# Performance work log

Hardware: AMD Instinct MI355X
Metric: run time of the kernel (lower is better)

## Reference

```python
import jax, jax.numpy as jnp
import numpy as np

B, T, D, H = 2, 2048, 1024, 16
HD = D // H
REG = 16
WIN = 256
ROPE_BASE = 10000.0


def _rope_cos_sin(t, hd):
    theta = 1.0 / (ROPE_BASE ** (jnp.arange(0, hd, 2, dtype=jnp.float32) / hd))  # [hd/2]
    idx_theta = jnp.arange(t, dtype=jnp.float32)[:, None] * theta[None, :]       # [T, hd/2]
    return jnp.cos(idx_theta), jnp.sin(idx_theta)


def _apply_rope(x, cos, sin):
    # x: [B, T, H, HD]
    xs = x.reshape(*x.shape[:-1], HD // 2, 2)
    x0, x1 = xs[..., 0], xs[..., 1]
    c = cos[None, :, None, :]
    s = sin[None, :, None, :]
    out = jnp.stack([x0 * c - x1 * s, x1 * c + x0 * s], axis=-1)
    return out.reshape(x.shape)


def _keep_mask(t):
    # Faithful to _build_attention_register_mask: True = attend (SDPA bool semantics).
    i = jnp.arange(t)[:, None]
    j = jnp.arange(t)[None, :]
    half = WIN // 2
    window_block = (i >= REG) & (j >= jnp.maximum(REG, i - half)) & (j <= i + half)
    blocked = (j < REG) | (i < REG) | window_block
    return ~blocked  # [T, T] bool


def setup_inputs() -> dict:
    key = jax.random.key(0)
    k1, k2, k3 = jax.random.split(key, 3)
    x = jax.random.normal(k1, (B, T, D), dtype=jnp.float32)
    w_attn = jax.random.normal(k2, (3 * D, D), dtype=jnp.float32) * 0.02  # torch Linear weight [out,in]
    w_proj = jax.random.normal(k3, (D, D), dtype=jnp.float32) * 0.02
    return {"x": x, "w_attn": w_attn, "w_proj": w_proj}


def reference(x, w_attn, w_proj):
    b, t, d = x.shape
    qkv = jnp.einsum('btd,ed->bte', x, w_attn)               # [B,T,3D]
    q, k, v = jnp.split(qkv, 3, axis=-1)
    q = q.reshape(b, t, H, HD)
    k = k.reshape(b, t, H, HD)
    v = v.reshape(b, t, H, HD)
    cos, sin = _rope_cos_sin(t, HD)
    q = _apply_rope(q, cos, sin)
    k = _apply_rope(k, cos, sin)
    q = q.transpose(0, 2, 1, 3)  # [B,H,T,HD]
    k = k.transpose(0, 2, 1, 3)
    v = v.transpose(0, 2, 1, 3)
    keep = _keep_mask(t)
    scores = jnp.einsum('bhqd,bhkd->bhqk', q, k) / jnp.sqrt(jnp.float32(HD))
    scores = jnp.where(keep[None, None], scores, -jnp.inf)
    # safe softmax (fully-masked rows -> 0, matching SDPA efficient backends)
    m = jnp.max(scores, axis=-1, keepdims=True)
    m = jnp.where(jnp.isfinite(m), m, 0.0)
    e = jnp.exp(scores - m)
    s = jnp.sum(e, axis=-1, keepdims=True)
    probs = e / jnp.maximum(s, 1e-20)
    y = jnp.einsum('bhqk,bhkd->bhqd', probs, v)
    y = y.transpose(0, 2, 1, 3).reshape(b, t, d)
    return jnp.einsum('btd,ed->bte', y, w_proj)
```

## Files before the change

### kernel.cpp

```cpp
#include <hip/hip_runtime.h>
#include <hip/hip_bf16.h>

#define DEV static __device__ __forceinline__

typedef __attribute__((ext_vector_type(8))) short bf16x8;
typedef __attribute__((ext_vector_type(4))) float f32x4;

#define MFMA16(a, b, c) __builtin_amdgcn_mfma_f32_16x16x32_bf16((a), (b), (c), 0, 0, 0)

#define B_ 2
#define T_ 2048
#define D_ 1024
#define H_ 16
#define HD_ 64
#define LOG2E 1.4426950408889634f

DEV short f2bf(float f) {
  union { float f; unsigned u; } w; w.f = f;
  unsigned u = w.u + 0x7fffu + ((w.u >> 16) & 1u);
  return (short)(u >> 16);
}

DEV void gld16(const void* g, void* l) {
  __builtin_amdgcn_global_load_lds(
      (const __attribute__((address_space(1))) void*)g,
      (__attribute__((address_space(3))) void*)l, 16, 0, 0);
}

#define XN 4194304
#define WAN 3145728
__global__ void cvt_k(const float* __restrict__ x, const float* __restrict__ wa,
                      const float* __restrict__ wp, short* __restrict__ xb,
                      short* __restrict__ wab, short* __restrict__ wpb) {
  size_t gi = ((size_t)blockIdx.x * 256 + threadIdx.x) * 8;
  const float* src; short* dst;
  if (gi < XN) { src = x + gi; dst = xb + gi; }
  else if (gi < XN + WAN) { src = wa + (gi - XN); dst = wab + (gi - XN); }
  else { src = wp + (gi - XN - WAN); dst = wpb + (gi - XN - WAN); }
  float4 a = *(const float4*)src;
  float4 b = *(const float4*)(src + 4);
  bf16x8 o;
  o[0] = f2bf(a.x); o[1] = f2bf(a.y); o[2] = f2bf(a.z); o[3] = f2bf(a.w);
  o[4] = f2bf(b.x); o[5] = f2bf(b.y); o[6] = f2bf(b.z); o[7] = f2bf(b.w);
  *(bf16x8*)dst = o;
}

__global__ void rope_table_k(float2* __restrict__ tab) {
  int i = blockIdx.x * 256 + threadIdx.x;
  if (i >= T_ * 32) return;
  int t = i >> 5, d = i & 31;
  float theta = powf(10000.0f, -(float)(2 * d) / 64.0f);
  float a = (float)t * theta;
  tab[i] = make_float2(cosf(a), sinf(a));
}

#define GEMM_CORE(Aptr, Bptr, KDIM)                                              \
  __shared__ short aT[128 * 64];                                                 \
  __shared__ short bT[128 * 64];                                                 \
  const int tid = threadIdx.x;                                                   \
  const int lane = tid & 63, w = tid >> 6;                                       \
  const int l15 = lane & 15, lg = lane >> 4;                                     \
  const int wr = w >> 1, wc = w & 1;                                             \
  const int mBase = blockIdx.y * 128, nBase = blockIdx.x * 128;                  \
  const int lrow = lane >> 3;                                                    \
  const int gch = (lane & 7) ^ lrow;                                             \
  const short* Asrc = (Aptr) + (size_t)(mBase + w * 32 + lrow) * (KDIM) + gch * 8;\
  const short* Bsrc = (Bptr) + (size_t)(nBase + w * 32 + lrow) * (KDIM) + gch * 8;\
  short* aDst = aT + w * 2048;                                                   \
  short* bDst = bT + w * 2048;                                                   \
  f32x4 acc[4][4];                                                               \
  _Pragma("unroll") for (int i = 0; i < 4; ++i)                                  \
  _Pragma("unroll") for (int j = 0; j < 4; ++j)                                  \
      acc[i][j] = (f32x4){0.f, 0.f, 0.f, 0.f};                                   \
  const int nk = (KDIM) / 64;                                                    \
  for (int kt = 0; kt < nk; ++kt) {                                              \
    if (kt) __syncthreads();                                                     \
    _Pragma("unroll") for (int p = 0; p < 4; ++p) {                              \
      gld16(Asrc + kt * 64 + p * 8 * (KDIM), aDst + p * 512);                    \
      gld16(Bsrc + kt * 64 + p * 8 * (KDIM), bDst + p * 512);                    \
    }                                                                            \
    __syncthreads();                \
    bf16x8 af[4][2], bfv[4][2];                                                  \
    _Pragma("unroll") for (int i = 0; i < 4; ++i)                                \
    _Pragma("unroll") for (int s = 0; s < 2; ++s) {                              \
      const int ra = wr * 64 + i * 16 + l15;                                     \
      const int rb = wc * 64 + i * 16 + l15;                                     \
      af[i][s] = *(const bf16x8*)&aT[ra * 64 + (((4 * s + lg) ^ (ra & 7)) * 8)]; \
      bfv[i][s] = *(const bf16x8*)&bT[rb * 64 + (((4 * s + lg) ^ (rb & 7)) * 8)];\
    }                                                                            \
    _Pragma("unroll") for (int mi = 0; mi < 4; ++mi)                             \
    _Pragma("unroll") for (int ni = 0; ni < 4; ++ni)                             \
    _Pragma("unroll") for (int s = 0; s < 2; ++s)                                \
        acc[mi][ni] = MFMA16(af[mi][s], bfv[ni][s], acc[mi][ni]);                \
  }

__global__ void gemm_qkv_k(const short* __restrict__ Xb, const short* __restrict__ Wb,
                           short* __restrict__ Q, short* __restrict__ Ko,
                           short* __restrict__ Vt, const float2* __restrict__ tab) {
  GEMM_CORE(Xb, Wb, 1024)

  const int sec = nBase >> 10;
#pragma unroll
  for (int mi = 0; mi < 4; ++mi) {
    const int m0 = mBase + wr * 64 + mi * 16 + lg * 4;
#pragma unroll
    for (int ni = 0; ni < 4; ++ni) {
      const int n = nBase + wc * 64 + ni * 16 + l15;
      const int hd = n & 63;
      const int h = (n >> 6) & 15;
      if (sec < 2) {
        short* dst = (sec == 0) ? Q : Ko;
        const float qscale = (sec == 0) ? (0.125f * LOG2E) : 1.0f;
#pragma unroll
        for (int r = 0; r < 4; ++r) {
          int m = m0 + r; int b = m >> 11; int t = m & 2047;
          float v = acc[mi][ni][r];
          float pv = __shfl_xor(v, 1);
          float2 cs = tab[t * 32 + (hd >> 1)];
          float o = (lane & 1) ? (v * cs.x + pv * cs.y) : (v * cs.x - pv * cs.y);
          o *= qscale;
          dst[(((size_t)b * H_ + h) * T_ + t) * HD_ + hd] = f2bf(o);
        }
      } else {
        int b = m0 >> 11; int t0 = m0 & 2047;
        short4 s4;
        s4.x = f2bf(acc[mi][ni][0]); s4.y = f2bf(acc[mi][ni][1]);
        s4.z = f2bf(acc[mi][ni][2]); s4.w = f2bf(acc[mi][ni][3]);
        *(short4*)&Vt[(((size_t)b * H_ + h) * HD_ + hd) * T_ + t0] = s4;
      }
    }
  }
}

__global__ void attn_k(const short* __restrict__ Qg, const short* __restrict__ Kg,
                       const short* __restrict__ Vg, short* __restrict__ Y) {
  __shared__ short kLds[64 * 72];
  __shared__ short vLds[64 * 72];
  __shared__ short pLds[64 * 72];
  const int tid = threadIdx.x;
  const int lane = tid & 63, w = tid >> 6;
  const int l15 = lane & 15, lg = lane >> 4;
  const int bid = blockIdx.x;
  const int wg = ((bid & 7) << 7) | (bid >> 3);
  const int qt = wg & 31, bh = wg >> 5;
  const int b = bh >> 4, h = bh & 15;
  const int q0 = qt * 64;
  const short* Qh = Qg + (size_t)bh * T_ * HD_;
  const short* Kh = Kg + (size_t)bh * T_ * HD_;
  const short* Vh = Vg + (size_t)bh * HD_ * T_;

  bf16x8 qa[2];
  {
    const int qrow = q0 + w * 16 + l15;
    qa[0] = *(const bf16x8*)&Qh[(size_t)qrow * HD_ + lg * 8];
    qa[1] = *(const bf16x8*)&Qh[(size_t)qrow * HD_ + 32 + lg * 8];
  }
  f32x4 o[4];
#pragma unroll
  for (int i = 0; i < 4; ++i) o[i] = (f32x4){0.f, 0.f, 0.f, 0.f};
  float lsum[4] = {0.f, 0.f, 0.f, 0.f};

  const int sRow = tid >> 3, sC = (tid & 7) * 8;
  bf16x8 kreg[2], vreg[2];
  auto issueLoad = [&](int kt) {
    const int k0 = kt * 64;
#pragma unroll
    for (int p = 0; p < 2; ++p) {
      const int row = sRow + p * 32;
      kreg[p] = *(const bf16x8*)&Kh[(size_t)(k0 + row) * HD_ + sC];
      vreg[p] = *(const bf16x8*)&Vh[(size_t)row * T_ + k0 + sC];
    }
  };
  auto inBand = [&](int kt) { const int k0 = kt * 64; return k0 >= q0 - 65 && k0 <= q0 + 65; };

  const int NT = T_ / 64;
  int kt = 0;
  while (kt < NT && inBand(kt)) ++kt;
  issueLoad(kt);

  while (kt < NT) {
    int ktn = kt + 1;
    while (ktn < NT && inBand(ktn)) ++ktn;

    __syncthreads();
#pragma unroll
    for (int p = 0; p < 2; ++p) {
      *(bf16x8*)&kLds[(sRow + p * 32) * 72 + sC] = kreg[p];
      *(bf16x8*)&vLds[(sRow + p * 32) * 72 + sC] = vreg[p];
    }
    if (ktn < NT) issueLoad(ktn);
    asm volatile("s_waitcnt lgkmcnt(0)" ::: "memory");
    __builtin_amdgcn_s_barrier();

    const int k0 = kt * 64;
    const bool clean = (q0 >= 16) && (k0 >= 16) &&
                       ((k0 + 63 < q0 - 128) || (k0 > q0 + 63 + 128));

    f32x4 s[4];
#pragma unroll
    for (int i = 0; i < 4; ++i) s[i] = (f32x4){0.f, 0.f, 0.f, 0.f};
#pragma unroll
    for (int nf = 0; nf < 4; ++nf)
#pragma unroll
      for (int ks = 0; ks < 2; ++ks) {
        bf16x8 kb = *(const bf16x8*)&kLds[(nf * 16 + l15) * 72 + ks * 32 + lg * 8];
        s[nf] = MFMA16(qa[ks], kb, s[nf]);
      }

    if (!clean) {
#pragma unroll
      for (int nf = 0; nf < 4; ++nf) {
        const int j = k0 + nf * 16 + l15;
#pragma unroll
        for (int r = 0; r < 4; ++r) {
          const int i = q0 + w * 16 + lg * 4 + r;
          const bool keep = (i >= 16) && (j >= 16) && ((j < i - 128) || (j > i + 128));
          if (!keep) s[nf][r] = -__builtin_inff();
        }
      }
    }

#pragma unroll
    for (int nf = 0; nf < 4; ++nf)
#pragma unroll
      for (int r = 0; r < 4; ++r) {
        float e = __builtin_amdgcn_exp2f(s[nf][r]);
        lsum[r] += e;
        pLds[(w * 16 + lg * 4 + r) * 72 + nf * 16 + l15] = f2bf(e);
      }
#pragma unroll
    for (int nf = 0; nf < 4; ++nf)
#pragma unroll
      for (int ks = 0; ks < 2; ++ks) {
        bf16x8 pa = *(const bf16x8*)&pLds[(w * 16 + l15) * 72 + ks * 32 + lg * 8];
        bf16x8 vb = *(const bf16x8*)&vLds[(nf * 16 + l15) * 72 + ks * 32 + lg * 8];
        o[nf] = MFMA16(pa, vb, o[nf]);
      }
    kt = ktn;
  }

  float rl[4];
#pragma unroll
  for (int r = 0; r < 4; ++r) {
    float v = lsum[r];
    v += __shfl_xor(v, 1);
    v += __shfl_xor(v, 2);
    v += __shfl_xor(v, 4);
    v += __shfl_xor(v, 8);
    rl[r] = 1.0f / fmaxf(v, 1e-20f);
  }
#pragma unroll
  for (int nf = 0; nf < 4; ++nf)
#pragma unroll
    for (int r = 0; r < 4; ++r) {
      const int t = q0 + w * 16 + lg * 4 + r;
      Y[((size_t)(b * T_ + t)) * D_ + h * HD_ + nf * 16 + l15] = f2bf(o[nf][r] * rl[r]);
    }
}

__global__ void gemm_proj_k(const short* __restrict__ Yg, const short* __restrict__ Wb,
                            float* __restrict__ Out) {
  GEMM_CORE(Yg, Wb, 1024)

#pragma unroll
  for (int mi = 0; mi < 4; ++mi)
#pragma unroll
    for (int ni = 0; ni < 4; ++ni)
#pragma unroll
      for (int r = 0; r < 4; ++r)
        Out[(size_t)(mBase + wr * 64 + mi * 16 + lg * 4 + r) * 1024 +
            nBase + wc * 64 + ni * 16 + l15] = acc[mi][ni][r];
}

extern "C" void kernel_launch(void* const* d_in, const int* in_sizes, int n_in,
                              void* d_out, int out_size, void* d_ws, size_t ws_size,
                              hipStream_t stream) {
  const float* x = (const float*)d_in[0];
  const float* w_attn = (const float*)d_in[1];
  const float* w_proj = (const float*)d_in[2];
  float* out = (float*)d_out;
  char* ws = (char*)d_ws;
  char* outc = (char*)d_out;
  short* Q   = (short*)(ws);
  short* K   = (short*)(ws + (size_t)8388608);
  short* Vt  = (short*)(ws + (size_t)16777216);
  short* Y   = (short*)(ws + (size_t)25165824);
  short* Wpb = (short*)(ws + (size_t)33554432);
  short* Xb   = (short*)(outc);
  short* Wab  = (short*)(outc + (size_t)8388608);
  float2* tab = (float2*)(outc + (size_t)14680064);

  cvt_k<<<dim3(4096), dim3(256), 0, stream>>>(x, w_attn, w_proj, Xb, Wab, Wpb);
  rope_table_k<<<dim3(256), dim3(256), 0, stream>>>(tab);
  gemm_qkv_k<<<dim3(24, 32), dim3(256), 0, stream>>>(Xb, Wab, Q, K, Vt, tab);
  attn_k<<<dim3(B_ * H_ * (T_ / 64)), dim3(256), 0, stream>>>(Q, K, Vt, Y);
  gemm_proj_k<<<dim3(8, 32), dim3(256), 0, stream>>>(Y, Wpb, out);
}
```

Measured before the change: 144.5 us.

## Process 128 query rows per attention block to reuse K/V tiles

Each attention workgroup now handles two 64-row query chunks, so every K/V tile staged in shared memory is used by both chunks and global K/V traffic per query drops by half. The launch grid is halved to match, and the band-skip test is narrowed so only tiles fully masked for both chunks are skipped; partly masked tiles are computed and masked instead. MFMA sections are wrapped in s_setprio raises, and launch bounds request two blocks per CU. The trade is more registers per thread, fewer workgroups to spread across CUs, and some extra masked tile work near the diagonal band.

Result: slower. 148.7 us (+2.9%).

```diff
diff --git a/kernel.cpp b/kernel.cpp
--- a/kernel.cpp
+++ b/kernel.cpp
@@ -132,8 +132,11 @@
   }
 }
 
-__global__ void attn_k(const short* __restrict__ Qg, const short* __restrict__ Kg,
-                       const short* __restrict__ Vg, short* __restrict__ Y) {
+#define QB 128
+__global__ __launch_bounds__(256, 2) void attn_k(const short* __restrict__ Qg,
+                                                 const short* __restrict__ Kg,
+                                                 const short* __restrict__ Vg,
+                                                 short* __restrict__ Y) {
   __shared__ short kLds[64 * 72];
   __shared__ short vLds[64 * 72];
   __shared__ short pLds[64 * 72];
@@ -141,24 +144,31 @@
   const int lane = tid & 63, w = tid >> 6;
   const int l15 = lane & 15, lg = lane >> 4;
   const int bid = blockIdx.x;
-  const int wg = ((bid & 7) << 7) | (bid >> 3);
-  const int qt = wg & 31, bh = wg >> 5;
+  const int wg = ((bid & 7) << 6) | (bid >> 3);
+  const int qt = wg & 15, bh = wg >> 4;
   const int b = bh >> 4, h = bh & 15;
-  const int q0 = qt * 64;
+  const int q0 = qt * QB;
   const short* Qh = Qg + (size_t)bh * T_ * HD_;
   const short* Kh = Kg + (size_t)bh * T_ * HD_;
   const short* Vh = Vg + (size_t)bh * HD_ * T_;
 
-  bf16x8 qa[2];
-  {
-    const int qrow = q0 + w * 16 + l15;
-    qa[0] = *(const bf16x8*)&Qh[(size_t)qrow * HD_ + lg * 8];
-    qa[1] = *(const bf16x8*)&Qh[(size_t)qrow * HD_ + 32 + lg * 8];
-  }
-  f32x4 o[4];
-#pragma unroll
-  for (int i = 0; i < 4; ++i) o[i] = (f32x4){0.f, 0.f, 0.f, 0.f};
-  float lsum[4] = {0.f, 0.f, 0.f, 0.f};
+  bf16x8 qa[2][2];
+#pragma unroll
+  for (int c = 0; c < 2; ++c) {
+    const int qrow = q0 + c * 64 + w * 16 + l15;
+    qa[c][0] = *(const bf16x8*)&Qh[(size_t)qrow * HD_ + lg * 8];
+    qa[c][1] = *(const bf16x8*)&Qh[(size_t)qrow * HD_ + 32 + lg * 8];
+  }
+  f32x4 o[2][4];
+#pragma unroll
+  for (int c = 0; c < 2; ++c)
+#pragma unroll
+    for (int i = 0; i < 4; ++i) o[c][i] = (f32x4){0.f, 0.f, 0.f, 0.f};
+  float lsum[2][4];
+#pragma unroll
+  for (int c = 0; c < 2; ++c)
+#pragma unroll
+    for (int r = 0; r < 4; ++r) lsum[c][r] = 0.f;
 
   const int sRow = tid >> 3, sC = (tid & 7) * 8;
   bf16x8 kreg[2], vreg[2];
@@ -171,7 +181,7 @@
       vreg[p] = *(const bf16x8*)&Vh[(size_t)row * T_ + k0 + sC];
     }
   };
-  auto inBand = [&](int kt) { const int k0 = kt * 64; return k0 >= q0 - 65 && k0 <= q0 + 65; };
+  auto inBand = [&](int kt) { const int k0 = kt * 64; return k0 >= q0 - 1 && k0 <= q0 + 65; };
 
   const int NT = T_ / 64;
   int kt = 0;
@@ -193,69 +203,81 @@
     __builtin_amdgcn_s_barrier();
 
     const int k0 = kt * 64;
-    const bool clean = (q0 >= 16) && (k0 >= 16) &&
-                       ((k0 + 63 < q0 - 128) || (k0 > q0 + 63 + 128));
-
-    f32x4 s[4];
-#pragma unroll
-    for (int i = 0; i < 4; ++i) s[i] = (f32x4){0.f, 0.f, 0.f, 0.f};
+#pragma unroll
+    for (int c = 0; c < 2; ++c) {
+      const int qc = q0 + c * 64;
+      const bool clean = (qc >= 16) && (k0 >= 16) &&
+                         ((k0 + 63 < qc - 128) || (k0 > qc + 63 + 128));
+
+      f32x4 s[4];
+#pragma unroll
+      for (int i = 0; i < 4; ++i) s[i] = (f32x4){0.f, 0.f, 0.f, 0.f};
+      __builtin_amdgcn_s_setprio(1);
+#pragma unroll
+      for (int nf = 0; nf < 4; ++nf)
+#pragma unroll
+        for (int ks = 0; ks < 2; ++ks) {
+          bf16x8 kb = *(const bf16x8*)&kLds[(nf * 16 + l15) * 72 + ks * 32 + lg * 8];
+          s[nf] = MFMA16(qa[c][ks], kb, s[nf]);
+        }
+      __builtin_amdgcn_s_setprio(0);
+
+      if (!clean) {
+#pragma unroll
+        for (int nf = 0; nf < 4; ++nf) {
+          const int j = k0 + nf * 16 + l15;
+#pragma unroll
+          for (int r = 0; r < 4; ++r) {
+            const int i = qc + w * 16 + lg * 4 + r;
+            const bool keep = (i >= 16) && (j >= 16) && ((j < i - 128) || (j > i + 128));
+            if (!keep) s[nf][r] = -__builtin_inff();
+          }
+        }
+      }
+
+#pragma unroll
+      for (int nf = 0; nf < 4; ++nf)
+#pragma unroll
+        for (int r = 0; r < 4; ++r) {
+          float e = __builtin_amdgcn_exp2f(s[nf][r]);
+          lsum[c][r] += e;
+          pLds[(w * 16 + lg * 4 + r) * 72 + nf * 16 + l15] = f2bf(e);
+        }
+      __builtin_amdgcn_s_setprio(1);
+#pragma unroll
+      for (int nf = 0; nf < 4; ++nf)
+#pragma unroll
+        for (int ks = 0; ks < 2; ++ks) {
+          bf16x8 pa = *(const bf16x8*)&pLds[(w * 16 + l15) * 72 + ks * 32 + lg * 8];
+          bf16x8 vb = *(const bf16x8*)&vLds[(nf * 16 + l15) * 72 + ks * 32 + lg * 8];
+          o[c][nf] = MFMA16(pa, vb, o[c][nf]);
+        }
+      __builtin_amdgcn_s_setprio(0);
+    }
+    kt = ktn;
+  }
+
+#pragma unroll
+  for (int c = 0; c < 2; ++c) {
+    float rl[4];
+#pragma unroll
+    for (int r = 0; r < 4; ++r) {
+      float v = lsum[c][r];
+      v += __shfl_xor(v, 1);
+      v += __shfl_xor(v, 2);
+      v += __shfl_xor(v, 4);
+      v += __shfl_xor(v, 8);
+      rl[r] = 1.0f / fmaxf(v, 1e-20f);
+    }
 #pragma unroll
     for (int nf = 0; nf < 4; ++nf)
 #pragma unroll
-      for (int ks = 0; ks < 2; ++ks) {
-        bf16x8 kb = *(const bf16x8*)&kLds[(nf * 16 + l15) * 72 + ks * 32 + lg * 8];
-        s[nf] = MFMA16(qa[ks], kb, s[nf]);
+      for (int r = 0; r < 4; ++r) {
+        const int t = q0 + c * 64 + w * 16 + lg * 4 + r;
+        Y[((size_t)(b * T_ + t)) * D_ + h * HD_ + nf * 16 + l15] =
+            f2bf(o[c][nf][r] * rl[r]);
       }
-
-    if (!clean) {
-#pragma unroll
-      for (int nf = 0; nf < 4; ++nf) {
-        const int j = k0 + nf * 16 + l15;
-#pragma unroll
-        for (int r = 0; r < 4; ++r) {
-          const int i = q0 + w * 16 + lg * 4 + r;
-          const bool keep = (i >= 16) && (j >= 16) && ((j < i - 128) || (j > i + 128));
-          if (!keep) s[nf][r] = -__builtin_inff();
-        }
-      }
-    }
-
-#pragma unroll
-    for (int nf = 0; nf < 4; ++nf)
-#pragma unroll
-      for (int r = 0; r < 4; ++r) {
-        float e = __builtin_amdgcn_exp2f(s[nf][r]);
-        lsum[r] += e;
-        pLds[(w * 16 + lg * 4 + r) * 72 + nf * 16 + l15] = f2bf(e);
-      }
-#pragma unroll
-    for (int nf = 0; nf < 4; ++nf)
-#pragma unroll
-      for (int ks = 0; ks < 2; ++ks) {
-        bf16x8 pa = *(const bf16x8*)&pLds[(w * 16 + l15) * 72 + ks * 32 + lg * 8];
-        bf16x8 vb = *(const bf16x8*)&vLds[(nf * 16 + l15) * 72 + ks * 32 + lg * 8];
-        o[nf] = MFMA16(pa, vb, o[nf]);
-      }
-    kt = ktn;
-  }
-
-  float rl[4];
-#pragma unroll
-  for (int r = 0; r < 4; ++r) {
-    float v = lsum[r];
-    v += __shfl_xor(v, 1);
-    v += __shfl_xor(v, 2);
-    v += __shfl_xor(v, 4);
-    v += __shfl_xor(v, 8);
-    rl[r] = 1.0f / fmaxf(v, 1e-20f);
-  }
-#pragma unroll
-  for (int nf = 0; nf < 4; ++nf)
-#pragma unroll
-    for (int r = 0; r < 4; ++r) {
-      const int t = q0 + w * 16 + lg * 4 + r;
-      Y[((size_t)(b * T_ + t)) * D_ + h * HD_ + nf * 16 + l15] = f2bf(o[nf][r] * rl[r]);
-    }
+  }
 }
 
 __global__ void gemm_proj_k(const short* __restrict__ Yg, const short* __restrict__ Wb,
@@ -293,6 +315,6 @@
   cvt_k<<<dim3(4096), dim3(256), 0, stream>>>(x, w_attn, w_proj, Xb, Wab, Wpb);
   rope_table_k<<<dim3(256), dim3(256), 0, stream>>>(tab);
   gemm_qkv_k<<<dim3(24, 32), dim3(256), 0, stream>>>(Xb, Wab, Q, K, Vt, tab);
-  attn_k<<<dim3(B_ * H_ * (T_ / 64)), dim3(256), 0, stream>>>(Q, K, Vt, Y);
+  attn_k<<<dim3(B_ * H_ * (T_ / QB)), dim3(256), 0, stream>>>(Q, K, Vt, Y);
   gemm_proj_k<<<dim3(8, 32), dim3(256), 0, stream>>>(Y, Wpb, out);
 }
```

## Compute transposed scores to keep P in registers and drop P LDS round-trip

Applied to the files above, without the earlier changes.

The attention kernel now computes S^T (K as the A operand, Q as the B operand), so each lane holds probabilities for one query row in the layout a 16x16x16 bf16 MFMA B operand needs. P then feeds the PV product straight from registers, which removes the pLds buffer and its write/read round trip. The K LDS tile gets an XOR swizzle to cut bank conflicts, and s_setprio is placed around the MFMA sections. The output is staged through LDS to produce coalesced 16-byte stores. The cost is twice as many PV MFMAs at half the K depth, plus an occupancy hint via launch bounds.

New measurement: 149.3 us. 1.03x slower.

```diff
diff --git a/kernel.cpp b/kernel.cpp
--- a/kernel.cpp
+++ b/kernel.cpp
@@ -4,9 +4,23 @@
 #define DEV static __device__ __forceinline__
 
 typedef __attribute__((ext_vector_type(8))) short bf16x8;
+typedef __attribute__((ext_vector_type(4))) short bf16x4;
 typedef __attribute__((ext_vector_type(4))) float f32x4;
 
 #define MFMA16(a, b, c) __builtin_amdgcn_mfma_f32_16x16x32_bf16((a), (b), (c), 0, 0, 0)
+
+DEV f32x4 pv_mfma(bf16x4 a, bf16x4 b, f32x4 c) {
+#if __has_builtin(__builtin_amdgcn_mfma_f32_16x16x16_bf16)
+  return __builtin_amdgcn_mfma_f32_16x16x16_bf16(a, b, c, 0, 0, 0);
+#elif __has_builtin(__builtin_amdgcn_mfma_f32_16x16x16bf16_1k)
+  return __builtin_amdgcn_mfma_f32_16x16x16bf16_1k(a, b, c, 0, 0, 0);
+#else
+  f32x4 d;
+  asm volatile("v_mfma_f32_16x16x16_bf16 %0, %1, %2, %3"
+               : "=v"(d) : "v"(a), "v"(b), "v"(c));
+  return d;
+#endif
+}
 
 #define B_ 2
 #define T_ 2048
@@ -132,11 +146,12 @@
   }
 }
 
-__global__ void attn_k(const short* __restrict__ Qg, const short* __restrict__ Kg,
-                       const short* __restrict__ Vg, short* __restrict__ Y) {
+__global__ __launch_bounds__(256, 4) void attn_k(const short* __restrict__ Qg,
+                                                 const short* __restrict__ Kg,
+                                                 const short* __restrict__ Vg,
+                                                 short* __restrict__ Y) {
   __shared__ short kLds[64 * 72];
   __shared__ short vLds[64 * 72];
-  __shared__ short pLds[64 * 72];
   const int tid = threadIdx.x;
   const int lane = tid & 63, w = tid >> 6;
   const int l15 = lane & 15, lg = lane >> 4;
@@ -149,16 +164,16 @@
   const short* Kh = Kg + (size_t)bh * T_ * HD_;
   const short* Vh = Vg + (size_t)bh * HD_ * T_;
 
-  bf16x8 qa[2];
+  bf16x8 qb[2];
   {
     const int qrow = q0 + w * 16 + l15;
-    qa[0] = *(const bf16x8*)&Qh[(size_t)qrow * HD_ + lg * 8];
-    qa[1] = *(const bf16x8*)&Qh[(size_t)qrow * HD_ + 32 + lg * 8];
-  }
-  f32x4 o[4];
-#pragma unroll
-  for (int i = 0; i < 4; ++i) o[i] = (f32x4){0.f, 0.f, 0.f, 0.f};
-  float lsum[4] = {0.f, 0.f, 0.f, 0.f};
+    qb[0] = *(const bf16x8*)&Qh[(size_t)qrow * HD_ + lg * 8];
+    qb[1] = *(const bf16x8*)&Qh[(size_t)qrow * HD_ + 32 + lg * 8];
+  }
+  f32x4 ot[4];
+#pragma unroll
+  for (int i = 0; i < 4; ++i) ot[i] = (f32x4){0.f, 0.f, 0.f, 0.f};
+  float lsum = 0.f;
 
   const int sRow = tid >> 3, sC = (tid & 7) * 8;
   bf16x8 kreg[2], vreg[2];
@@ -185,8 +200,9 @@
     __syncthreads();
 #pragma unroll
     for (int p = 0; p < 2; ++p) {
-      *(bf16x8*)&kLds[(sRow + p * 32) * 72 + sC] = kreg[p];
-      *(bf16x8*)&vLds[(sRow + p * 32) * 72 + sC] = vreg[p];
+      const int row = sRow + p * 32;
+      *(bf16x8*)&kLds[row * 72 + (((tid & 7) ^ (row & 7)) * 8)] = kreg[p];
+      *(bf16x8*)&vLds[row * 72 + sC] = vreg[p];
     }
     if (ktn < NT) issueLoad(ktn);
     asm volatile("s_waitcnt lgkmcnt(0)" ::: "memory");
@@ -199,63 +215,73 @@
     f32x4 s[4];
 #pragma unroll
     for (int i = 0; i < 4; ++i) s[i] = (f32x4){0.f, 0.f, 0.f, 0.f};
+    __builtin_amdgcn_s_setprio(1);
 #pragma unroll
     for (int nf = 0; nf < 4; ++nf)
 #pragma unroll
       for (int ks = 0; ks < 2; ++ks) {
-        bf16x8 kb = *(const bf16x8*)&kLds[(nf * 16 + l15) * 72 + ks * 32 + lg * 8];
-        s[nf] = MFMA16(qa[ks], kb, s[nf]);
+        const int row = nf * 16 + l15;
+        bf16x8 ka = *(const bf16x8*)&kLds[row * 72 + (((ks * 4 + lg) ^ (row & 7)) * 8)];
+        s[nf] = MFMA16(ka, qb[ks], s[nf]);
       }
-
-    if (!clean) {
-#pragma unroll
-      for (int nf = 0; nf < 4; ++nf) {
-        const int j = k0 + nf * 16 + l15;
-#pragma unroll
-        for (int r = 0; r < 4; ++r) {
-          const int i = q0 + w * 16 + lg * 4 + r;
-          const bool keep = (i >= 16) && (j >= 16) && ((j < i - 128) || (j > i + 128));
+    __builtin_amdgcn_s_setprio(0);
+
+    const int i_q = q0 + w * 16 + l15;
+    bf16x4 pf[4];
+#pragma unroll
+    for (int nf = 0; nf < 4; ++nf)
+#pragma unroll
+      for (int r = 0; r < 4; ++r) {
+        if (!clean) {
+          const int j = k0 + nf * 16 + lg * 4 + r;
+          const bool keep = (i_q >= 16) && (j >= 16) &&
+                            ((j < i_q - 128) || (j > i_q + 128));
           if (!keep) s[nf][r] = -__builtin_inff();
         }
+        float e = __builtin_amdgcn_exp2f(s[nf][r]);
+        lsum += e;
+        pf[nf][r] = f2bf(e);
       }
+
+    __builtin_amdgcn_s_setprio(1);
+#pragma unroll
+    for (int kk = 0; kk < 4; ++kk) {
+      bf16x4 va[4];
+#pragma unroll
+      for (int dt = 0; dt < 4; ++dt)
+        va[dt] = *(const bf16x4*)&vLds[(dt * 16 + l15) * 72 + kk * 16 + lg * 4];
+#pragma unroll
+      for (int dt = 0; dt < 4; ++dt)
+        ot[dt] = pv_mfma(va[dt], pf[kk], ot[dt]);
     }
-
-#pragma unroll
-    for (int nf = 0; nf < 4; ++nf)
-#pragma unroll
-      for (int r = 0; r < 4; ++r) {
-        float e = __builtin_amdgcn_exp2f(s[nf][r]);
-        lsum[r] += e;
-        pLds[(w * 16 + lg * 4 + r) * 72 + nf * 16 + l15] = f2bf(e);
-      }
-#pragma unroll
-    for (int nf = 0; nf < 4; ++nf)
-#pragma unroll
-      for (int ks = 0; ks < 2; ++ks) {
-        bf16x8 pa = *(const bf16x8*)&pLds[(w * 16 + l15) * 72 + ks * 32 + lg * 8];
-        bf16x8 vb = *(const bf16x8*)&vLds[(nf * 16 + l15) * 72 + ks * 32 + lg * 8];
-        o[nf] = MFMA16(pa, vb, o[nf]);
-      }
+    __builtin_amdgcn_s_setprio(0);
     kt = ktn;
   }
 
-  float rl[4];
-#pragma unroll
-  for (int r = 0; r < 4; ++r) {
-    float v = lsum[r];
-    v += __shfl_xor(v, 1);
-    v += __shfl_xor(v, 2);
-    v += __shfl_xor(v, 4);
-    v += __shfl_xor(v, 8);
-    rl[r] = 1.0f / fmaxf(v, 1e-20f);
-  }
-#pragma unroll
-  for (int nf = 0; nf < 4; ++nf)
-#pragma unroll
-    for (int r = 0; r < 4; ++r) {
-      const int t = q0 + w * 16 + lg * 4 + r;
-      Y[((size_t)(b * T_ + t)) * D_ + h * HD_ + nf * 16 + l15] = f2bf(o[nf][r] * rl[r]);
-    }
+  float l = lsum;
+  l += __shfl_xor(l, 16);
+  l += __shfl_xor(l, 32);
+  const float rl = 1.0f / fmaxf(l, 1e-20f);
+
+  __syncthreads();
+  short* tl = kLds + w * (16 * 72);
+#pragma unroll
+  for (int dt = 0; dt < 4; ++dt) {
+    short4 s4;
+    s4.x = f2bf(ot[dt][0] * rl);
+    s4.y = f2bf(ot[dt][1] * rl);
+    s4.z = f2bf(ot[dt][2] * rl);
+    s4.w = f2bf(ot[dt][3] * rl);
+    *(short4*)&tl[l15 * 72 + dt * 16 + lg * 4] = s4;
+  }
+  const int rr = lane >> 3, cc = (lane & 7) * 8;
+#pragma unroll
+  for (int hf = 0; hf < 2; ++hf) {
+    const int row = hf * 8 + rr;
+    bf16x8 v = *(const bf16x8*)&tl[row * 72 + cc];
+    const int t = q0 + w * 16 + row;
+    *(bf16x8*)&Y[((size_t)(b * T_ + t)) * D_ + h * HD_ + cc] = v;
+  }
 }
 
 __global__ void gemm_proj_k(const short* __restrict__ Yg, const short* __restrict__ Wb,
```

## Share each K/V tile across two 64-row query groups per attention block

Applied to the files above, without the earlier changes.

Each attention workgroup now covers 128 query rows with 8 waves in two groups of four, instead of 64 rows with 4 waves. Each K/V tile staged in LDS is reused by both groups, which halves global K/V traffic per query. Tiles are skipped only when both groups are fully masked, and each group skips its own masked band. This trades halved grid size and some idle waves on band tiles for better reuse.

Result: slower. 148.8 us (+3.0%).

```diff
diff --git a/kernel.cpp b/kernel.cpp
--- a/kernel.cpp
+++ b/kernel.cpp
@@ -132,26 +132,32 @@
   }
 }
 
-__global__ void attn_k(const short* __restrict__ Qg, const short* __restrict__ Kg,
-                       const short* __restrict__ Vg, short* __restrict__ Y) {
+#define QBLK 128
+__global__ __launch_bounds__(512, 8) void attn_k(const short* __restrict__ Qg,
+                                                 const short* __restrict__ Kg,
+                                                 const short* __restrict__ Vg,
+                                                 short* __restrict__ Y) {
   __shared__ short kLds[64 * 72];
   __shared__ short vLds[64 * 72];
-  __shared__ short pLds[64 * 72];
+  __shared__ short pLds[2 * 64 * 72];
   const int tid = threadIdx.x;
   const int lane = tid & 63, w = tid >> 6;
+  const int g = w >> 2, wl = w & 3;
   const int l15 = lane & 15, lg = lane >> 4;
   const int bid = blockIdx.x;
-  const int wg = ((bid & 7) << 7) | (bid >> 3);
-  const int qt = wg & 31, bh = wg >> 5;
+  const int wg = ((bid & 7) << 6) | (bid >> 3);
+  const int qt = wg & 15, bh = wg >> 4;
   const int b = bh >> 4, h = bh & 15;
-  const int q0 = qt * 64;
+  const int q0 = qt * QBLK;
+  const int qg = q0 + g * 64;
   const short* Qh = Qg + (size_t)bh * T_ * HD_;
   const short* Kh = Kg + (size_t)bh * T_ * HD_;
   const short* Vh = Vg + (size_t)bh * HD_ * T_;
+  short* pl = pLds + g * 4608;
 
   bf16x8 qa[2];
   {
-    const int qrow = q0 + w * 16 + l15;
+    const int qrow = qg + wl * 16 + l15;
     qa[0] = *(const bf16x8*)&Qh[(size_t)qrow * HD_ + lg * 8];
     qa[1] = *(const bf16x8*)&Qh[(size_t)qrow * HD_ + 32 + lg * 8];
   }
@@ -161,81 +167,76 @@
   float lsum[4] = {0.f, 0.f, 0.f, 0.f};
 
   const int sRow = tid >> 3, sC = (tid & 7) * 8;
-  bf16x8 kreg[2], vreg[2];
+  bf16x8 kreg, vreg;
   auto issueLoad = [&](int kt) {
     const int k0 = kt * 64;
-#pragma unroll
-    for (int p = 0; p < 2; ++p) {
-      const int row = sRow + p * 32;
-      kreg[p] = *(const bf16x8*)&Kh[(size_t)(k0 + row) * HD_ + sC];
-      vreg[p] = *(const bf16x8*)&Vh[(size_t)row * T_ + k0 + sC];
-    }
+    kreg = *(const bf16x8*)&Kh[(size_t)(k0 + sRow) * HD_ + sC];
+    vreg = *(const bf16x8*)&Vh[(size_t)sRow * T_ + k0 + sC];
   };
-  auto inBand = [&](int kt) { const int k0 = kt * 64; return k0 >= q0 - 65 && k0 <= q0 + 65; };
+  auto bothBanned = [&](int kt) { const int k0 = kt * 64; return k0 >= q0 - 1 && k0 <= q0 + 65; };
 
   const int NT = T_ / 64;
   int kt = 0;
-  while (kt < NT && inBand(kt)) ++kt;
+  while (kt < NT && bothBanned(kt)) ++kt;
   issueLoad(kt);
 
   while (kt < NT) {
     int ktn = kt + 1;
-    while (ktn < NT && inBand(ktn)) ++ktn;
+    while (ktn < NT && bothBanned(ktn)) ++ktn;
 
     __syncthreads();
-#pragma unroll
-    for (int p = 0; p < 2; ++p) {
-      *(bf16x8*)&kLds[(sRow + p * 32) * 72 + sC] = kreg[p];
-      *(bf16x8*)&vLds[(sRow + p * 32) * 72 + sC] = vreg[p];
-    }
+    *(bf16x8*)&kLds[sRow * 72 + sC] = kreg;
+    *(bf16x8*)&vLds[sRow * 72 + sC] = vreg;
     if (ktn < NT) issueLoad(ktn);
     asm volatile("s_waitcnt lgkmcnt(0)" ::: "memory");
     __builtin_amdgcn_s_barrier();
 
     const int k0 = kt * 64;
-    const bool clean = (q0 >= 16) && (k0 >= 16) &&
-                       ((k0 + 63 < q0 - 128) || (k0 > q0 + 63 + 128));
-
-    f32x4 s[4];
-#pragma unroll
-    for (int i = 0; i < 4; ++i) s[i] = (f32x4){0.f, 0.f, 0.f, 0.f};
-#pragma unroll
-    for (int nf = 0; nf < 4; ++nf)
-#pragma unroll
-      for (int ks = 0; ks < 2; ++ks) {
-        bf16x8 kb = *(const bf16x8*)&kLds[(nf * 16 + l15) * 72 + ks * 32 + lg * 8];
-        s[nf] = MFMA16(qa[ks], kb, s[nf]);
+    if (!(k0 >= qg - 65 && k0 <= qg + 65)) {
+      const bool clean = (qg >= 16) && (k0 >= 16) &&
+                         ((k0 + 63 < qg - 128) || (k0 > qg + 63 + 128));
+
+      f32x4 s[4];
+#pragma unroll
+      for (int i = 0; i < 4; ++i) s[i] = (f32x4){0.f, 0.f, 0.f, 0.f};
+#pragma unroll
+      for (int nf = 0; nf < 4; ++nf)
+#pragma unroll
+        for (int ks = 0; ks < 2; ++ks) {
+          bf16x8 kb = *(const bf16x8*)&kLds[(nf * 16 + l15) * 72 + ks * 32 + lg * 8];
+          s[nf] = MFMA16(qa[ks], kb, s[nf]);
+        }
+
+      if (!clean) {
+#pragma unroll
+        for (int nf = 0; nf < 4; ++nf) {
+          const int j = k0 + nf * 16 + l15;
+#pragma unroll
+          for (int r = 0; r < 4; ++r) {
+            const int i = qg + wl * 16 + lg * 4 + r;
+            const bool keep = (i >= 16) && (j >= 16) && ((j < i - 128) || (j > i + 128));
+            if (!keep) s[nf][r] = -__builtin_inff();
+          }
+        }
       }
 
-    if (!clean) {
-#pragma unroll
-      for (int nf = 0; nf < 4; ++nf) {
-        const int j = k0 + nf * 16 + l15;
+#pragma unroll
+      for (int nf = 0; nf < 4; ++nf)
 #pragma unroll
         for (int r = 0; r < 4; ++r) {
-          const int i = q0 + w * 16 + lg * 4 + r;
-          const bool keep = (i >= 16) && (j >= 16) && ((j < i - 128) || (j > i + 128));
-          if (!keep) s[nf][r] = -__builtin_inff();
-        }
-      }
+          float e = __builtin_amdgcn_exp2f(s[nf][r]);
+          lsum[r] += e;
+          pl[(wl * 16 + lg * 4 + r) * 72 + nf * 16 + l15] = f2bf(e);
+        }
+#pragma unroll
+      for (int nf = 0; nf < 4; ++nf)
+#pragma unroll
+        for (int ks = 0; ks < 2; ++ks) {
+          bf16x8 pa = *(const bf16x8*)&pl[(wl * 16 + l15) * 72 + ks * 32 + lg * 8];
+          bf16x8 vb = *(const bf16x8*)&vLds[(nf * 16 + l15) * 72 + ks * 32 + lg * 8];
+          o[nf] = MFMA16(pa, vb, o[nf]);
+        }
     }
-
-#pragma unroll
-    for (int nf = 0; nf < 4; ++nf)
-#pragma unroll
-      for (int r = 0; r < 4; ++r) {
-        float e = __builtin_amdgcn_exp2f(s[nf][r]);
-        lsum[r] += e;
-        pLds[(w * 16 + lg * 4 + r) * 72 + nf * 16 + l15] = f2bf(e);
-      }
-#pragma unroll
-    for (int nf = 0; nf < 4; ++nf)
-#pragma unroll
-      for (int ks = 0; ks < 2; ++ks) {
-        bf16x8 pa = *(const bf16x8*)&pLds[(w * 16 + l15) * 72 + ks * 32 + lg * 8];
-        bf16x8 vb = *(const bf16x8*)&vLds[(nf * 16 + l15) * 72 + ks * 32 + lg * 8];
-        o[nf] = MFMA16(pa, vb, o[nf]);
-      }
     kt = ktn;
   }
 
@@ -253,7 +254,7 @@
   for (int nf = 0; nf < 4; ++nf)
 #pragma unroll
     for (int r = 0; r < 4; ++r) {
-      const int t = q0 + w * 16 + lg * 4 + r;
+      const int t = qg + wl * 16 + lg * 4 + r;
       Y[((size_t)(b * T_ + t)) * D_ + h * HD_ + nf * 16 + l15] = f2bf(o[nf][r] * rl[r]);
     }
 }
@@ -293,6 +294,6 @@
   cvt_k<<<dim3(4096), dim3(256), 0, stream>>>(x, w_attn, w_proj, Xb, Wab, Wpb);
   rope_table_k<<<dim3(256), dim3(256), 0, stream>>>(tab);
   gemm_qkv_k<<<dim3(24, 32), dim3(256), 0, stream>>>(Xb, Wab, Q, K, Vt, tab);
-  attn_k<<<dim3(B_ * H_ * (T_ / 64)), dim3(256), 0, stream>>>(Q, K, Vt, Y);
+  attn_k<<<dim3(B_ * H_ * (T_ / QBLK)), dim3(512), 0, stream>>>(Q, K, Vt, Y);
   gemm_proj_k<<<dim3(8, 32), dim3(256), 0, stream>>>(Y, Wpb, out);
 }
```
